# Optimization experiments

Measured on AMD Instinct MI355X. Metric: run time of the kernel, lower is better.

Reference implementation:

```python
import math
import jax, jax.numpy as jnp
import numpy as np

N_NODES = 100000
N_EDGES = 3200000
D = 128
H = 8
DK = D // H


def setup_inputs() -> dict:
    key = jax.random.key(0)
    ks = jax.random.split(key, 12)
    s = 1.0 / math.sqrt(D)
    return {
        "feat": jax.random.normal(ks[0], (N_NODES, D), jnp.float32),
        "Wk": jax.random.normal(ks[1], (D, D), jnp.float32) * s,
        "bk": jax.random.normal(ks[2], (D,), jnp.float32) * s,
        "Wq": jax.random.normal(ks[3], (D, D), jnp.float32) * s,
        "bq": jax.random.normal(ks[4], (D,), jnp.float32) * s,
        "Wv": jax.random.normal(ks[5], (D, D), jnp.float32) * s,
        "bv": jax.random.normal(ks[6], (D,), jnp.float32) * s,
        "w_att": jax.random.normal(ks[7], (H, DK, DK), jnp.float32) * (1.0 / math.sqrt(DK)),
        "w_msg": jax.random.normal(ks[8], (H, DK, DK), jnp.float32) * (1.0 / math.sqrt(DK)),
        "mu": jax.random.uniform(ks[9], (1,), jnp.float32, 0.5, 1.5),
        "src": jax.random.randint(ks[10], (N_EDGES,), 0, N_NODES, jnp.int32),
        "dst": jax.random.randint(ks[11], (N_EDGES,), 0, N_NODES, jnp.int32),
    }


def reference(feat, Wk, bk, Wq, bq, Wv, bv, w_att, w_msg, mu, src, dst):
    N = feat.shape[0]
    # node projections, per-head relation transforms
    k = (feat @ Wk.T + bk).reshape(N, H, DK)            # (N,H,dk)
    v = (feat @ Wv.T + bv).reshape(N, H, DK)
    q = (feat @ Wq.T + bq).reshape(N, H, DK)
    k = jnp.einsum('nhi,hij->nhj', k, w_att)
    v = jnp.einsum('nhi,hij->nhj', v, w_msg)
    # edge-wise q (dst) . k (src) attention logits
    logits = jnp.einsum('ehd,ehd->eh', q[dst], k[src])  # (E,H)
    logits = logits * (mu[0] / math.sqrt(DK))
    # segment softmax over incoming edges of each dst node
    m = jax.ops.segment_max(logits, dst, num_segments=N)   # (N,H)
    ex = jnp.exp(logits - m[dst])
    denom = jax.ops.segment_sum(ex, dst, num_segments=N)   # (N,H)
    attn = ex / denom[dst]                                  # (E,H)
    # weighted message aggregation
    msg = v[src] * attn[..., None]                          # (E,H,dk)
    h = jax.ops.segment_sum(msg, dst, num_segments=N)       # (N,H,dk)
    return h.reshape(N, H * DK)
```

## Files before the change

### kernel.cpp

```cpp
#include <hip/hip_runtime.h>
#include <hip/hip_bf16.h>
#include <stdint.h>

#define DD 128
#define HH 8
#define DKK 16

#define BSHIFT 7
#define BNODES (1 << BSHIFT)
#define SC_EPT 16

typedef __attribute__((ext_vector_type(8))) short bf16x8;
typedef __attribute__((ext_vector_type(4))) float f32x4;

__device__ __forceinline__ float bfhi2f(unsigned u) {
  union { unsigned i; float f; } c; c.i = u & 0xFFFF0000u; return c.f;
}
__device__ __forceinline__ float bflo2f(unsigned u) {
  union { unsigned i; float f; } c; c.i = u << 16; return c.f;
}
__device__ __forceinline__ unsigned short f2bf(float f) {
  __hip_bfloat16 b = __float2bfloat16(f);
  return *reinterpret_cast<unsigned short*>(&b);
}

__global__ __launch_bounds__(256) void prep_weights(
    const float* __restrict__ Wq, const float* __restrict__ bq,
    const float* __restrict__ Wk, const float* __restrict__ bk,
    const float* __restrict__ Wv, const float* __restrict__ bv,
    const float* __restrict__ w_att, const float* __restrict__ w_msg,
    const float* __restrict__ mu,
    unsigned short* __restrict__ WcatT, float* __restrict__ bcat) {
  int gid = blockIdx.x * blockDim.x + threadIdx.x;
  if (gid >= DD * 384) return;
  int f = gid / 384;
  int o = gid % 384;
  float scale = mu[0] * 0.25f;
  float w;
  if (o < 128) {
    w = Wq[o * DD + f] * scale;
  } else if (o < 256) {
    int c = o - 128, h = c >> 4, j = c & 15;
    float s = 0.f;
#pragma unroll
    for (int i = 0; i < 16; ++i)
      s += Wk[(h * 16 + i) * DD + f] * w_att[h * 256 + i * 16 + j];
    w = s;
  } else {
    int c = o - 256, h = c >> 4, j = c & 15;
    float s = 0.f;
#pragma unroll
    for (int i = 0; i < 16; ++i)
      s += Wv[(h * 16 + i) * DD + f] * w_msg[h * 256 + i * 16 + j];
    w = s;
  }
  WcatT[(size_t)o * DD + f] = f2bf(w);
  if (f == 0) {
    float b;
    if (o < 128) {
      b = bq[o] * scale;
    } else if (o < 256) {
      int c = o - 128, h = c >> 4, j = c & 15;
      float s = 0.f;
#pragma unroll
      for (int i = 0; i < 16; ++i)
        s += bk[h * 16 + i] * w_att[h * 256 + i * 16 + j];
      b = s;
    } else {
      int c = o - 256, h = c >> 4, j = c & 15;
      float s = 0.f;
#pragma unroll
      for (int i = 0; i < 16; ++i)
        s += bv[h * 16 + i] * w_msg[h * 256 + i * 16 + j];
      b = s;
    }
    bcat[o] = b;
  }
}

__global__ __launch_bounds__(256) void proj_gemm(
    const float* __restrict__ feat, const unsigned short* __restrict__ WcatT,
    const float* __restrict__ bcat, float* __restrict__ Q,
    __hip_bfloat16* __restrict__ KV, int N) {
  int row0 = blockIdx.x * 64;
  int wave = threadIdx.x >> 6, lane = threadIdx.x & 63;
  int lrow = lane & 15, lk = lane >> 4;
  int arow = row0 + wave * 16 + lrow;
  const float* ap = feat + (size_t)(arow < N ? arow : 0) * DD;

  bf16x8 a[4];
#pragma unroll
  for (int ks = 0; ks < 4; ++ks) {
    float4 a0 = *(const float4*)(ap + ks * 32 + lk * 8);
    float4 a1 = *(const float4*)(ap + ks * 32 + lk * 8 + 4);
    union { bf16x8 v; unsigned short s[8]; } u;
    u.s[0] = f2bf(a0.x); u.s[1] = f2bf(a0.y);
    u.s[2] = f2bf(a0.z); u.s[3] = f2bf(a0.w);
    u.s[4] = f2bf(a1.x); u.s[5] = f2bf(a1.y);
    u.s[6] = f2bf(a1.z); u.s[7] = f2bf(a1.w);
    a[ks] = u.v;
  }

  int outrow = row0 + wave * 16 + lk * 4;
#pragma unroll
  for (int nf = 0; nf < 24; ++nf) {
    f32x4 acc = (f32x4){0.f, 0.f, 0.f, 0.f};
#pragma unroll
    for (int ks = 0; ks < 4; ++ks) {
      bf16x8 b = *(const bf16x8*)(WcatT + (size_t)(nf * 16 + lrow) * DD +
                                  ks * 32 + lk * 8);
      acc = __builtin_amdgcn_mfma_f32_16x16x32_bf16(a[ks], b, acc, 0, 0, 0);
    }
    int col = nf * 16 + lrow;
    float bias = bcat[col];
#pragma unroll
    for (int r = 0; r < 4; ++r) {
      int grow = outrow + r;
      if (grow >= N) continue;
      float c = acc[r] + bias;
      if (col < 128) {
        Q[(size_t)grow * DD + col] = c;
      } else if (col < 256) {
        int cc = col - 128;
        KV[(size_t)grow * 256 + (cc >> 4) * 32 + (cc & 15)] =
            __float2bfloat16(c);
      } else {
        int cc = col - 256;
        KV[(size_t)grow * 256 + (cc >> 4) * 32 + 16 + (cc & 15)] =
            __float2bfloat16(c);
      }
    }
  }
}

__global__ __launch_bounds__(256) void bucket_hist(
    const int* __restrict__ dst, int* __restrict__ bucket_count, int E,
    int NB) {
  __shared__ int h[1024];
  int tid = threadIdx.x;
  for (int i = tid; i < NB; i += 256) h[i] = 0;
  __syncthreads();
  for (int e = blockIdx.x * blockDim.x + tid; e < E;
       e += gridDim.x * blockDim.x)
    atomicAdd(&h[dst[e] >> BSHIFT], 1);
  __syncthreads();
  for (int i = tid; i < NB; i += 256)
    if (h[i]) atomicAdd(&bucket_count[i], h[i]);
}

__global__ __launch_bounds__(64) void bucket_scan(
    const int* __restrict__ bucket_count, int* __restrict__ bucket_base,
    int* __restrict__ bucket_cursor, int NB) {
  int lane = threadIdx.x;
  int running = 0;
  for (int c0 = 0; c0 < NB; c0 += 64) {
    int idx = c0 + lane;
    int v = (idx < NB) ? bucket_count[idx] : 0;
    int s = v;
#pragma unroll
    for (int off = 1; off < 64; off <<= 1) {
      int t = __shfl_up(s, off);
      if (lane >= off) s += t;
    }
    int excl = running + s - v;
    if (idx < NB) {
      bucket_base[idx] = excl;
      bucket_cursor[idx] = excl;
    }
    running += __shfl(s, 63);
  }
}

__global__ __launch_bounds__(256) void bucket_scatter(
    const int* __restrict__ src, const int* __restrict__ dst,
    int* __restrict__ bucket_cursor, unsigned* __restrict__ ebuf, int E,
    int NB) {
  __shared__ int h[1024];
  __shared__ int cur[1024];
  int tid = threadIdx.x;
  int base0 = blockIdx.x * (256 * SC_EPT);
  for (int i = tid; i < NB; i += 256) h[i] = 0;
  __syncthreads();
  int myd[SC_EPT], mys[SC_EPT];
#pragma unroll
  for (int i = 0; i < SC_EPT; ++i) {
    int e = base0 + i * 256 + tid;
    if (e < E) {
      myd[i] = dst[e];
      mys[i] = src[e];
      atomicAdd(&h[myd[i] >> BSHIFT], 1);
    } else {
      myd[i] = -1;
    }
  }
  __syncthreads();
  for (int i = tid; i < NB; i += 256)
    cur[i] = h[i] ? atomicAdd(&bucket_cursor[i], h[i]) : 0;
  __syncthreads();
#pragma unroll
  for (int i = 0; i < SC_EPT; ++i) {
    if (myd[i] >= 0) {
      int b = myd[i] >> BSHIFT;
      int p = atomicAdd(&cur[b], 1);
      ebuf[p] = ((unsigned)(myd[i] & (BNODES - 1)) << 17) | (unsigned)mys[i];
    }
  }
}

__global__ __launch_bounds__(256) void bucket_to_csr(
    const unsigned* __restrict__ ebuf, const int* __restrict__ bucket_base,
    const int* __restrict__ bucket_count, int* __restrict__ rowptr,
    int* __restrict__ deg, int* __restrict__ esrc, int N) {
  __shared__ int h[BNODES];
  __shared__ int sc[BNODES];
  __shared__ int cur[BNODES];
  int b = blockIdx.x;
  int tid = threadIdx.x;
  int start = bucket_base[b];
  int cnt = bucket_count[b];
  if (tid < BNODES) h[tid] = 0;
  __syncthreads();
  for (int i = tid; i < cnt; i += 256)
    atomicAdd(&h[ebuf[start + i] >> 17], 1);
  __syncthreads();
  if (tid < BNODES) sc[tid] = h[tid];
  __syncthreads();
  for (int off = 1; off < BNODES; off <<= 1) {
    int t = 0;
    if (tid < BNODES && tid >= off) t = sc[tid - off];
    __syncthreads();
    if (tid < BNODES) sc[tid] += t;
    __syncthreads();
  }
  if (tid < BNODES) {
    int excl = sc[tid] - h[tid];
    int node = b * BNODES + tid;
    if (node < N) {
      rowptr[node] = start + excl;
      deg[node] = h[tid];
    }
    cur[tid] = excl;
  }
  __syncthreads();
  for (int i = tid; i < cnt; i += 256) {
    unsigned u = ebuf[start + i];
    int p = atomicAdd(&cur[u >> 17], 1);
    esrc[start + p] = (int)(u & 0x1FFFFu);
  }
}

__global__ __launch_bounds__(256) void node_aggregate(
    const int* __restrict__ esrc, const int* __restrict__ rowptr,
    const int* __restrict__ deg, const float* __restrict__ Q,
    const __hip_bfloat16* __restrict__ KV,
    float* __restrict__ out, int N) {
  int n = blockIdx.x * 4 + (threadIdx.x >> 6);
  if (n >= N) return;
  int lane = threadIdx.x & 63;
  int h = lane & 7;
  int p = lane >> 3;

  float q[16];
#pragma unroll
  for (int i = 0; i < 4; ++i) {
    float4 t = *(const float4*)(Q + (size_t)n * DD + h * DKK + i * 4);
    q[i * 4 + 0] = t.x; q[i * 4 + 1] = t.y;
    q[i * 4 + 2] = t.z; q[i * 4 + 3] = t.w;
  }
  int row = rowptr[n];
  int dg = deg[n];

  float acc[16];
#pragma unroll
  for (int j = 0; j < 16; ++j) acc[j] = 0.f;
  float den = 0.f;

  const unsigned short* KVu = (const unsigned short*)KV;

  for (int base = 0; base < dg; base += 64) {
    int myid = (base + lane < dg) ? esrc[row + base + lane] : 0;
    int cnt = min(64, dg - base);
    int iters = (cnt + 7) >> 3;
#pragma unroll 2
    for (int i = 0; i < iters; ++i) {
      int slot = i * 8 + p;
      int s = __shfl(myid, slot);
      float m = (base + slot < dg) ? 1.f : 0.f;
      const uint4* kvp = (const uint4*)(KVu + (size_t)s * 256 + h * 32);
      uint4 k0 = kvp[0], k1 = kvp[1];
      float dot;
      dot = q[0] * bflo2f(k0.x);
      dot = fmaf(q[1], bfhi2f(k0.x), dot);
      dot = fmaf(q[2], bflo2f(k0.y), dot);
      dot = fmaf(q[3], bfhi2f(k0.y), dot);
      dot = fmaf(q[4], bflo2f(k0.z), dot);
      dot = fmaf(q[5], bfhi2f(k0.z), dot);
      dot = fmaf(q[6], bflo2f(k0.w), dot);
      dot = fmaf(q[7], bfhi2f(k0.w), dot);
      dot = fmaf(q[8], bflo2f(k1.x), dot);
      dot = fmaf(q[9], bfhi2f(k1.x), dot);
      dot = fmaf(q[10], bflo2f(k1.y), dot);
      dot = fmaf(q[11], bfhi2f(k1.y), dot);
      dot = fmaf(q[12], bflo2f(k1.z), dot);
      dot = fmaf(q[13], bfhi2f(k1.z), dot);
      dot = fmaf(q[14], bflo2f(k1.w), dot);
      dot = fmaf(q[15], bfhi2f(k1.w), dot);
      float ex = m * __expf(fminf(dot, 80.f));
      den += ex;
      uint4 v0 = kvp[2], v1 = kvp[3];
      acc[0] = fmaf(ex, bflo2f(v0.x), acc[0]);
      acc[1] = fmaf(ex, bfhi2f(v0.x), acc[1]);
      acc[2] = fmaf(ex, bflo2f(v0.y), acc[2]);
      acc[3] = fmaf(ex, bfhi2f(v0.y), acc[3]);
      acc[4] = fmaf(ex, bflo2f(v0.z), acc[4]);
      acc[5] = fmaf(ex, bfhi2f(v0.z), acc[5]);
      acc[6] = fmaf(ex, bflo2f(v0.w), acc[6]);
      acc[7] = fmaf(ex, bfhi2f(v0.w), acc[7]);
      acc[8] = fmaf(ex, bflo2f(v1.x), acc[8]);
      acc[9] = fmaf(ex, bfhi2f(v1.x), acc[9]);
      acc[10] = fmaf(ex, bflo2f(v1.y), acc[10]);
      acc[11] = fmaf(ex, bfhi2f(v1.y), acc[11]);
      acc[12] = fmaf(ex, bflo2f(v1.z), acc[12]);
      acc[13] = fmaf(ex, bfhi2f(v1.z), acc[13]);
      acc[14] = fmaf(ex, bflo2f(v1.w), acc[14]);
      acc[15] = fmaf(ex, bfhi2f(v1.w), acc[15]);
    }
  }

#pragma unroll
  for (int j = 0; j < 16; ++j) {
    acc[j] += __shfl_xor(acc[j], 8);
    acc[j] += __shfl_xor(acc[j], 16);
    acc[j] += __shfl_xor(acc[j], 32);
  }
  den += __shfl_xor(den, 8);
  den += __shfl_xor(den, 16);
  den += __shfl_xor(den, 32);

  if (p == 0) {
    float inv = (dg > 0 && den > 0.f) ? 1.0f / den : 0.f;
#pragma unroll
    for (int i = 0; i < 4; ++i) {
      float4 o = make_float4(acc[i * 4 + 0] * inv, acc[i * 4 + 1] * inv,
                             acc[i * 4 + 2] * inv, acc[i * 4 + 3] * inv);
      *(float4*)(out + (size_t)n * DD + h * DKK + i * 4) = o;
    }
  }
}

extern "C" void kernel_launch(void* const* d_in, const int* in_sizes, int n_in,
                              void* d_out, int out_size, void* d_ws,
                              size_t ws_size, hipStream_t stream) {
  const float* feat = (const float*)d_in[0];
  const float* Wk = (const float*)d_in[1];
  const float* bk = (const float*)d_in[2];
  const float* Wq = (const float*)d_in[3];
  const float* bq = (const float*)d_in[4];
  const float* Wv = (const float*)d_in[5];
  const float* bv = (const float*)d_in[6];
  const float* w_att = (const float*)d_in[7];
  const float* w_msg = (const float*)d_in[8];
  const float* mu = (const float*)d_in[9];
  const int* src = (const int*)d_in[10];
  const int* dst = (const int*)d_in[11];

  int N = in_sizes[0] / DD;
  int E = in_sizes[10];
  int NB = (N + BNODES - 1) >> BSHIFT;

  char* ws = (char*)d_ws;
  unsigned short* WcatT = (unsigned short*)ws; ws += (size_t)DD * 384 * 2;
  float* bcat = (float*)ws; ws += 384 * 4;
  ws = (char*)(((uintptr_t)ws + 255) & ~(uintptr_t)255);
  float* Q = (float*)ws; ws += (size_t)N * DD * 4;
  __hip_bfloat16* KV = (__hip_bfloat16*)ws; ws += (size_t)N * 256 * 2;
  int* deg = (int*)ws; ws += (size_t)N * 4;
  int* rowptr = (int*)ws; ws += (size_t)N * 4;
  int* bucket_count = (int*)ws; ws += 1024 * 4;
  int* bucket_base = (int*)ws; ws += 1024 * 4;
  int* bucket_cursor = (int*)ws; ws += 1024 * 4;
  ws = (char*)(((uintptr_t)ws + 255) & ~(uintptr_t)255);
  unsigned* ebuf = (unsigned*)ws; ws += (size_t)E * 4;
  int* esrc = (int*)ws; ws += (size_t)E * 4;

  hipMemsetAsync(bucket_count, 0, 1024 * 4, stream);

  prep_weights<<<(DD * 384 + 255) / 256, 256, 0, stream>>>(
      Wq, bq, Wk, bk, Wv, bv, w_att, w_msg, mu, WcatT, bcat);

  proj_gemm<<<(N + 63) / 64, 256, 0, stream>>>(feat, WcatT, bcat, Q, KV, N);

  bucket_hist<<<256, 256, 0, stream>>>(dst, bucket_count, E, NB);
  bucket_scan<<<1, 64, 0, stream>>>(bucket_count, bucket_base, bucket_cursor,
                                    NB);
  int sc_blocks = (E + 256 * SC_EPT - 1) / (256 * SC_EPT);
  bucket_scatter<<<sc_blocks, 256, 0, stream>>>(src, dst, bucket_cursor, ebuf,
                                                E, NB);
  bucket_to_csr<<<NB, 256, 0, stream>>>(ebuf, bucket_base, bucket_count,
                                        rowptr, deg, esrc, N);

  node_aggregate<<<(N + 3) / 4, 256, 0, stream>>>(esrc, rowptr, deg, Q, KV,
                                                  (float*)d_out, N);
}
```

Baseline: 427.4 us.

## Quantize V to int8 per node-head with bf16 scale to shrink gather traffic

Adds a quantize_v kernel that converts each node-head's 16 V values to offset-int8 with a per-group bf16 scale. K (bf16) and the quantized V are packed into a 48-byte per-head record in a 384-byte row, with scales in a separate array. The aggregation kernel dequantizes on the fly by accumulating ex*scale times the raw bytes, then subtracts the 128 offset via a running sum of ex*scale. The goal is to cut random-gather bytes per edge from 64 to about 50. The cost is an extra kernel, an extra scale load per edge, and lower precision in V.

```diff
diff --git a/kernel.cpp b/kernel.cpp
--- a/kernel.cpp
+++ b/kernel.cpp
@@ -81,7 +81,8 @@
 __global__ __launch_bounds__(256) void proj_gemm(
     const float* __restrict__ feat, const unsigned short* __restrict__ WcatT,
     const float* __restrict__ bcat, float* __restrict__ Q,
-    __hip_bfloat16* __restrict__ KV, int N) {
+    __hip_bfloat16* __restrict__ Vb, unsigned char* __restrict__ KVrow,
+    int N) {
   int row0 = blockIdx.x * 64;
   int wave = threadIdx.x >> 6, lane = threadIdx.x & 63;
   int lrow = lane & 15, lk = lane >> 4;
@@ -121,16 +122,48 @@
       if (col < 128) {
         Q[(size_t)grow * DD + col] = c;
       } else if (col < 256) {
-        int cc = col - 128;
-        KV[(size_t)grow * 256 + (cc >> 4) * 32 + (cc & 15)] =
+        int cc = col - 128, h = cc >> 4, d = cc & 15;
+        *(__hip_bfloat16*)(KVrow + (size_t)grow * 384 + h * 48 + d * 2) =
             __float2bfloat16(c);
       } else {
-        int cc = col - 256;
-        KV[(size_t)grow * 256 + (cc >> 4) * 32 + 16 + (cc & 15)] =
-            __float2bfloat16(c);
+        Vb[(size_t)grow * DD + (col - 256)] = __float2bfloat16(c);
       }
     }
   }
+}
+
+__global__ __launch_bounds__(256) void quantize_v(
+    const __hip_bfloat16* __restrict__ Vb, unsigned char* __restrict__ KVrow,
+    unsigned short* __restrict__ S, int NH) {
+  int g = blockIdx.x * 256 + threadIdx.x;
+  if (g >= NH) return;
+  const unsigned* vp = (const unsigned*)Vb + (size_t)g * 8;
+  float v[16];
+#pragma unroll
+  for (int w = 0; w < 8; ++w) {
+    unsigned u = vp[w];
+    v[w * 2] = bflo2f(u); v[w * 2 + 1] = bfhi2f(u);
+  }
+  float mv = 0.f;
+#pragma unroll
+  for (int j = 0; j < 16; ++j) mv = fmaxf(mv, fabsf(v[j]));
+  float iv = (mv > 0.f) ? 127.f / mv : 0.f;
+  unsigned outw[4];
+#pragma unroll
+  for (int w = 0; w < 4; ++w) {
+    unsigned pv = 0;
+#pragma unroll
+    for (int b = 0; b < 4; ++b) {
+      int qv = (int)rintf(v[w * 4 + b] * iv) + 128;
+      qv = qv < 0 ? 0 : (qv > 255 ? 255 : qv);
+      pv |= (unsigned)qv << (8 * b);
+    }
+    outw[w] = pv;
+  }
+  int node = g >> 3, h = g & 7;
+  *(uint4*)(KVrow + (size_t)node * 384 + h * 48 + 32) =
+      make_uint4(outw[0], outw[1], outw[2], outw[3]);
+  S[g] = f2bf(mv / 127.f);
 }
 
 __global__ __launch_bounds__(256) void bucket_hist(
@@ -252,7 +285,8 @@
 __global__ __launch_bounds__(256) void node_aggregate(
     const int* __restrict__ esrc, const int* __restrict__ rowptr,
     const int* __restrict__ deg, const float* __restrict__ Q,
-    const __hip_bfloat16* __restrict__ KV,
+    const unsigned char* __restrict__ KVrow,
+    const unsigned short* __restrict__ S,
     float* __restrict__ out, int N) {
   int n = blockIdx.x * 4 + (threadIdx.x >> 6);
   if (n >= N) return;
@@ -273,9 +307,7 @@
   float acc[16];
 #pragma unroll
   for (int j = 0; j < 16; ++j) acc[j] = 0.f;
-  float den = 0.f;
-
-  const unsigned short* KVu = (const unsigned short*)KV;
+  float den = 0.f, evsum = 0.f;
 
   for (int base = 0; base < dg; base += 64) {
     int myid = (base + lane < dg) ? esrc[row + base + lane] : 0;
@@ -286,8 +318,11 @@
       int slot = i * 8 + p;
       int s = __shfl(myid, slot);
       float m = (base + slot < dg) ? 1.f : 0.f;
-      const uint4* kvp = (const uint4*)(KVu + (size_t)s * 256 + h * 32);
-      uint4 k0 = kvp[0], k1 = kvp[1];
+      const unsigned char* rp = KVrow + (size_t)s * 384 + h * 48;
+      uint4 k0 = *(const uint4*)rp;
+      uint4 k1 = *(const uint4*)(rp + 16);
+      uint4 vq = *(const uint4*)(rp + 32);
+      float sV = bflo2f((unsigned)S[(size_t)s * 8 + h]);
       float dot;
       dot = q[0] * bflo2f(k0.x);
       dot = fmaf(q[1], bfhi2f(k0.x), dot);
@@ -307,23 +342,24 @@
       dot = fmaf(q[15], bfhi2f(k1.w), dot);
       float ex = m * __expf(fminf(dot, 80.f));
       den += ex;
-      uint4 v0 = kvp[2], v1 = kvp[3];
-      acc[0] = fmaf(ex, bflo2f(v0.x), acc[0]);
-      acc[1] = fmaf(ex, bfhi2f(v0.x), acc[1]);
-      acc[2] = fmaf(ex, bflo2f(v0.y), acc[2]);
-      acc[3] = fmaf(ex, bfhi2f(v0.y), acc[3]);
-      acc[4] = fmaf(ex, bflo2f(v0.z), acc[4]);
-      acc[5] = fmaf(ex, bfhi2f(v0.z), acc[5]);
-      acc[6] = fmaf(ex, bflo2f(v0.w), acc[6]);
-      acc[7] = fmaf(ex, bfhi2f(v0.w), acc[7]);
-      acc[8] = fmaf(ex, bflo2f(v1.x), acc[8]);
-      acc[9] = fmaf(ex, bfhi2f(v1.x), acc[9]);
-      acc[10] = fmaf(ex, bflo2f(v1.y), acc[10]);
-      acc[11] = fmaf(ex, bfhi2f(v1.y), acc[11]);
-      acc[12] = fmaf(ex, bflo2f(v1.z), acc[12]);
-      acc[13] = fmaf(ex, bfhi2f(v1.z), acc[13]);
-      acc[14] = fmaf(ex, bflo2f(v1.w), acc[14]);
-      acc[15] = fmaf(ex, bfhi2f(v1.w), acc[15]);
+      float evs = ex * sV;
+      evsum += evs;
+      acc[0] = fmaf(evs, (float)(vq.x & 255), acc[0]);
+      acc[1] = fmaf(evs, (float)((vq.x >> 8) & 255), acc[1]);
+      acc[2] = fmaf(evs, (float)((vq.x >> 16) & 255), acc[2]);
+      acc[3] = fmaf(evs, (float)(vq.x >> 24), acc[3]);
+      acc[4] = fmaf(evs, (float)(vq.y & 255), acc[4]);
+      acc[5] = fmaf(evs, (float)((vq.y >> 8) & 255), acc[5]);
+      acc[6] = fmaf(evs, (float)((vq.y >> 16) & 255), acc[6]);
+      acc[7] = fmaf(evs, (float)(vq.y >> 24), acc[7]);
+      acc[8] = fmaf(evs, (float)(vq.z & 255), acc[8]);
+      acc[9] = fmaf(evs, (float)((vq.z >> 8) & 255), acc[9]);
+      acc[10] = fmaf(evs, (float)((vq.z >> 16) & 255), acc[10]);
+      acc[11] = fmaf(evs, (float)(vq.z >> 24), acc[11]);
+      acc[12] = fmaf(evs, (float)(vq.w & 255), acc[12]);
+      acc[13] = fmaf(evs, (float)((vq.w >> 8) & 255), acc[13]);
+      acc[14] = fmaf(evs, (float)((vq.w >> 16) & 255), acc[14]);
+      acc[15] = fmaf(evs, (float)(vq.w >> 24), acc[15]);
     }
   }
 
@@ -336,13 +372,19 @@
   den += __shfl_xor(den, 8);
   den += __shfl_xor(den, 16);
   den += __shfl_xor(den, 32);
+  evsum += __shfl_xor(evsum, 8);
+  evsum += __shfl_xor(evsum, 16);
+  evsum += __shfl_xor(evsum, 32);
 
   if (p == 0) {
     float inv = (dg > 0 && den > 0.f) ? 1.0f / den : 0.f;
+    float corr = 128.f * evsum;
 #pragma unroll
     for (int i = 0; i < 4; ++i) {
-      float4 o = make_float4(acc[i * 4 + 0] * inv, acc[i * 4 + 1] * inv,
-                             acc[i * 4 + 2] * inv, acc[i * 4 + 3] * inv);
+      float4 o = make_float4((acc[i * 4 + 0] - corr) * inv,
+                             (acc[i * 4 + 1] - corr) * inv,
+                             (acc[i * 4 + 2] - corr) * inv,
+                             (acc[i * 4 + 3] - corr) * inv);
       *(float4*)(out + (size_t)n * DD + h * DKK + i * 4) = o;
     }
   }
@@ -373,7 +415,11 @@
   float* bcat = (float*)ws; ws += 384 * 4;
   ws = (char*)(((uintptr_t)ws + 255) & ~(uintptr_t)255);
   float* Q = (float*)ws; ws += (size_t)N * DD * 4;
-  __hip_bfloat16* KV = (__hip_bfloat16*)ws; ws += (size_t)N * 256 * 2;
+  __hip_bfloat16* Vb = (__hip_bfloat16*)ws; ws += (size_t)N * DD * 2;
+  unsigned char* KVrow = (unsigned char*)ws; ws += (size_t)N * 384;
+  ws = (char*)(((uintptr_t)ws + 255) & ~(uintptr_t)255);
+  unsigned short* S = (unsigned short*)ws; ws += (size_t)N * HH * 2;
+  ws = (char*)(((uintptr_t)ws + 255) & ~(uintptr_t)255);
   int* deg = (int*)ws; ws += (size_t)N * 4;
   int* rowptr = (int*)ws; ws += (size_t)N * 4;
   int* bucket_count = (int*)ws; ws += 1024 * 4;
@@ -388,7 +434,10 @@
   prep_weights<<<(DD * 384 + 255) / 256, 256, 0, stream>>>(
       Wq, bq, Wk, bk, Wv, bv, w_att, w_msg, mu, WcatT, bcat);
 
-  proj_gemm<<<(N + 63) / 64, 256, 0, stream>>>(feat, WcatT, bcat, Q, KV, N);
+  proj_gemm<<<(N + 63) / 64, 256, 0, stream>>>(feat, WcatT, bcat, Q, Vb,
+                                               KVrow, N);
+
+  quantize_v<<<(N * HH + 255) / 256, 256, 0, stream>>>(Vb, KVrow, S, N * HH);
 
   bucket_hist<<<256, 256, 0, stream>>>(dst, bucket_count, E, NB);
   bucket_scan<<<1, 64, 0, stream>>>(bucket_count, bucket_base, bucket_cursor,
@@ -399,6 +448,6 @@
   bucket_to_csr<<<NB, 256, 0, stream>>>(ebuf, bucket_base, bucket_count,
                                         rowptr, deg, esrc, N);
 
-  node_aggregate<<<(N + 3) / 4, 256, 0, stream>>>(esrc, rowptr, deg, Q, KV,
-                                                  (float*)d_out, N);
-}
+  node_aggregate<<<(N + 3) / 4, 256, 0, stream>>>(esrc, rowptr, deg, Q, KVrow,
+                                                  S, (float*)d_out, N);
+}
```

Measured after the change: 414.6 us. -3.0%, faster.
